# Kernel tuning notes

Hardware: AMD Instinct MI355X
Metric: run time of the kernel (lower is better)

Reference implementation:

```python
import jax, jax.numpy as jnp
import numpy as np

DIM, HEADS = 1536, 12
HD = DIM // HEADS            # 128 head dim
C = HD // 2                  # 64 complex (pair) dim
C0 = C - 2 * (C // 3)        # 22 (temporal axis)
C1 = C // 3                  # 21 (each spatial axis)
MAX_POS = 1024
F_, H_, W_ = 9, 22, 22
SEQ = F_ * H_ * W_           # 4356
NCLASS = 2
EPS = 1e-6


def _rope_tables():
    # Wan rope_params: theta = 10000, per-axis half-dims C0, C1, C1.
    def ang(half):
        inv = 1.0 / (10000.0 ** (np.arange(0, 2 * half, 2) / (2 * half)))
        return np.outer(np.arange(MAX_POS), inv)
    a = np.concatenate([ang(C0), ang(C1), ang(C1)], axis=1)  # [MAX_POS, C]
    return jnp.asarray(np.cos(a), jnp.float32), jnp.asarray(np.sin(a), jnp.float32)


def setup_inputs() -> dict:
    key = jax.random.key(0)
    ks = jax.random.split(key, 6)
    s = 1.0 / np.sqrt(DIM)
    def lin(k):
        k1, k2 = jax.random.split(k)
        return (jax.random.uniform(k1, (DIM, DIM), jnp.float32, -s, s),
                jax.random.uniform(k2, (DIM,), jnp.float32, -s, s))
    Wq, bq = lin(ks[0]); Wk, bk = lin(ks[1]); Wv, bv = lin(ks[2]); Wo, bo = lin(ks[3])
    fc, fs = _rope_tables()
    masks = (jax.random.uniform(ks[4], (NCLASS, H_ * W_)) < 0.5).astype(jnp.float32)
    x = jax.random.normal(ks[5], (1, SEQ, DIM), jnp.float32)
    return {"x": x, "Wq": Wq, "bq": bq, "Wk": Wk, "bk": bk, "Wv": Wv, "bv": bv,
            "Wo": Wo, "bo": bo, "gq": jnp.ones((DIM,), jnp.float32),
            "gk": jnp.ones((DIM,), jnp.float32), "freqs_cos": fc, "freqs_sin": fs,
            "ref_target_masks": masks, "f": F_, "h": H_, "w": W_}


def _rmsnorm(x, g):
    return x * jax.lax.rsqrt(jnp.mean(x * x, axis=-1, keepdims=True) + EPS) * g


def _grid_cs(tab, f, h, w):
    # per-position (f,h,w) rope table -> [f*h*w, C]
    p0 = jnp.broadcast_to(tab[:f, None, None, :C0], (f, h, w, C0))
    p1 = jnp.broadcast_to(tab[None, :h, None, C0:C0 + C1], (f, h, w, C1))
    p2 = jnp.broadcast_to(tab[None, None, :w, C0 + C1:], (f, h, w, C1))
    return jnp.concatenate([p0, p1, p2], axis=-1).reshape(f * h * w, C)


def _rope(x, cos, sin):
    # x: [b,s,n,d]; pairs are interleaved along d (view_as_complex semantics)
    b, s, n, d = x.shape
    xr = x.reshape(b, s, n, d // 2, 2)
    a, bi = xr[..., 0], xr[..., 1]
    cos = cos[None, :, None, :]
    sin = sin[None, :, None, :]
    out = jnp.stack([a * cos - bi * sin, a * sin + bi * cos], axis=-1)
    return out.reshape(b, s, n, d)


def reference(x, Wq, bq, Wk, bk, Wv, bv, Wo, bo, gq, gk, freqs_cos, freqs_sin,
              ref_target_masks, f, h, w):
    b, s, _ = x.shape
    n, d = HEADS, HD
    q = _rmsnorm(x @ Wq.T + bq, gq).reshape(b, s, n, d)
    k = _rmsnorm(x @ Wk.T + bk, gk).reshape(b, s, n, d)
    v = (x @ Wv.T + bv).reshape(b, s, n, d)
    cos = _grid_cs(freqs_cos, f, h, w)
    sin = _grid_cs(freqs_sin, f, h, w)
    q = _rope(q, cos, sin)
    k = _rope(k, cos, sin)
    scale = 1.0 / np.sqrt(d).astype(np.float32)
    # full (window_size == (-1,-1)) attention; seq_lens == s so k_lens mask is identity
    scores = jnp.einsum('bsnd,btnd->bnst', q, k) * scale
    p = jax.nn.softmax(scores, axis=-1)
    o = jnp.einsum('bnst,btnd->bsnd', p, v).reshape(b, s, n * d)
    out = o @ Wo.T + bo
    # aux attention map vs reference-frame keys (first h*w spatial tokens), no-grad path
    xs = h * w
    ref_k = k[:, :xs]
    s2 = jnp.einsum('bsnd,btnd->bnst', q * scale, ref_k)
    p2 = jax.nn.softmax(s2, axis=-1)                       # [b,n,s,xs]
    m = ref_target_masks                                   # [c,xs]
    maps = jnp.einsum('bnst,ct->cbns', p2, m) / jnp.sum(m, axis=-1)[:, None, None, None]
    attn_map = maps.mean(axis=2).reshape(-1, s)            # mean over heads -> [c*b, s]
    return out, attn_map
```

## Files before the change

### kernel.cpp

```cpp
#include <hip/hip_runtime.h>
#include <hip/hip_bf16.h>
#include <math.h>

constexpr int SEQ   = 4356;
constexpr int DIM   = 1536;
constexpr int HEADS = 12;
constexpr int HD    = 128;
constexpr int CH    = 64;
constexpr int C0c   = 22;
constexpr int C1c   = 21;
constexpr int WWc   = 22;
constexpr int HHWW  = 484;
constexpr int XS    = 484;
constexpr int KVB   = 64;
constexpr int NT    = (SEQ + KVB - 1) / KVB;
constexpr int SEQP  = NT * KVB;
constexpr size_t SD = (size_t)SEQ * DIM;

typedef float f32x4 __attribute__((ext_vector_type(4)));
typedef short bf16x8 __attribute__((ext_vector_type(8)));
typedef short bf16x4 __attribute__((ext_vector_type(4)));

__device__ inline unsigned short f2bf(float f) {
  union { float f; unsigned u; } x; x.f = f;
  return (unsigned short)((x.u + 0x7FFFu + ((x.u >> 16) & 1u)) >> 16);
}

#define GLD16(g, l)                                                                        \
  __builtin_amdgcn_global_load_lds((const __attribute__((address_space(1))) unsigned*)    \
                                       (const void*)(g),                                  \
                                   (__attribute__((address_space(3))) unsigned*)(void*)(l),\
                                   16, 0, 0)

__global__ __launch_bounds__(256) void prep_kernel(const float* __restrict__ mask,
                                                   float* __restrict__ amap,
                                                   float* __restrict__ cnt,
                                                   float4* __restrict__ msk4) {
  int t = threadIdx.x;
  for (int i = t; i < 2 * SEQ; i += 256) amap[i] = 0.f;
  for (int i = t; i < 512; i += 256) {
    float4 v;
    v.x = (i < XS) ? mask[i] : 0.f;
    v.y = (i < XS) ? mask[XS + i] : 0.f;
    v.z = (i < XS) ? 1.f : 0.f;
    v.w = 0.f;
    msk4[i] = v;
  }
  float c0 = 0.f, c1 = 0.f;
  for (int i = t; i < XS; i += 256) { c0 += mask[i]; c1 += mask[XS + i]; }
  __shared__ float red0[256];
  __shared__ float red1[256];
  red0[t] = c0; red1[t] = c1;
  __syncthreads();
  for (int off = 128; off > 0; off >>= 1) {
    if (t < off) { red0[t] += red0[t + off]; red1[t] += red1[t + off]; }
    __syncthreads();
  }
  if (t == 0) { cnt[0] = red0[0]; cnt[1] = red1[0]; }
}

__global__ __launch_bounds__(256) void padzero(unsigned short* __restrict__ vt) {
  const int pad = SEQP - SEQ;
  const int total = DIM * pad;
  for (int i = blockIdx.x * 256 + threadIdx.x; i < total; i += gridDim.x * 256) {
    const int d = i / pad, c = i - d * pad;
    vt[(size_t)d * SEQP + SEQ + c] = 0;
  }
}

__global__ __launch_bounds__(256) void to_bf16(const float* __restrict__ in,
                                               unsigned short* __restrict__ out, int n4) {
  for (int i = blockIdx.x * 256 + threadIdx.x; i < n4; i += gridDim.x * 256) {
    const float4 v = ((const float4*)in)[i];
    ushort4 o;
    o.x = f2bf(v.x); o.y = f2bf(v.y); o.z = f2bf(v.z); o.w = f2bf(v.w);
    ((ushort4*)out)[i] = o;
  }
}

__global__ __launch_bounds__(256) void to_bf16_w(const float* __restrict__ W0, const float* __restrict__ W1,
                                                 const float* __restrict__ W2, const float* __restrict__ W3,
                                                 unsigned short* __restrict__ o0, unsigned short* __restrict__ o1,
                                                 unsigned short* __restrict__ o2, unsigned short* __restrict__ o3,
                                                 int n4) {
  const int z = blockIdx.z;
  const float* in = (z == 0) ? W0 : (z == 1) ? W1 : (z == 2) ? W2 : W3;
  unsigned short* out = (z == 0) ? o0 : (z == 1) ? o1 : (z == 2) ? o2 : o3;
  for (int i = blockIdx.x * 256 + threadIdx.x; i < n4; i += gridDim.x * 256) {
    const float4 v = ((const float4*)in)[i];
    ushort4 o;
    o.x = f2bf(v.x); o.y = f2bf(v.y); o.z = f2bf(v.z); o.w = f2bf(v.w);
    ((ushort4*)out)[i] = o;
  }
}

__global__ __launch_bounds__(256) void gemm_qkv(const unsigned short* __restrict__ A,
                                                const unsigned short* __restrict__ B0,
                                                const unsigned short* __restrict__ B1,
                                                const unsigned short* __restrict__ B2,
                                                const float* __restrict__ bq,
                                                const float* __restrict__ bk,
                                                const float* __restrict__ bv,
                                                float* __restrict__ o0,
                                                float* __restrict__ o1,
                                                unsigned short* __restrict__ vtout,
                                                int M) {
  __shared__ unsigned short As[128 * 64];
  __shared__ unsigned short Bs[128 * 64];
  const int z = blockIdx.z;
  const unsigned short* B = (z == 0) ? B0 : (z == 1) ? B1 : B2;
  const float* bias = (z == 0) ? bq : (z == 1) ? bk : bv;
  const int t    = threadIdx.x;
  const int lane = t & 63;
  const int w    = t >> 6;
  const int wr   = w >> 1, wc = w & 1;
  const int bm = blockIdx.x * 128, bn = blockIdx.y * 128;
  const int lq = lane & 15, lg = lane >> 4;
  f32x4 acc[4][4] = {};
  for (int k0 = 0; k0 < DIM; k0 += 64) {
#pragma unroll
    for (int i = 0; i < 4; ++i) {
      const int idx = i * 256 + t;
      const int row = idx >> 3;
      const int c8  = (idx & 7) * 8;
      const int ga  = min(bm + row, M - 1);
      GLD16(A + (size_t)ga * DIM + k0 + c8, As + idx * 8);
      const int gb  = bn + row;
      GLD16(B + (size_t)gb * DIM + k0 + c8, Bs + idx * 8);
    }
    __syncthreads();
#pragma unroll
    for (int kk = 0; kk < 2; ++kk) {
      bf16x8 af[4], bf[4];
#pragma unroll
      for (int m = 0; m < 4; ++m)
        af[m] = *(const bf16x8*)(As + (wr * 64 + m * 16 + lq) * 64 + kk * 32 + lg * 8);
#pragma unroll
      for (int n = 0; n < 4; ++n)
        bf[n] = *(const bf16x8*)(Bs + (wc * 64 + n * 16 + lq) * 64 + kk * 32 + lg * 8);
#pragma unroll
      for (int m = 0; m < 4; ++m)
#pragma unroll
        for (int n = 0; n < 4; ++n)
          acc[m][n] = __builtin_amdgcn_mfma_f32_16x16x32_bf16(af[m], bf[n], acc[m][n], 0, 0, 0);
    }
    __syncthreads();
  }
#pragma unroll
  for (int n = 0; n < 4; ++n) {
    const int col = bn + wc * 64 + n * 16 + lq;
    const float bv2 = bias[col];
#pragma unroll
    for (int m = 0; m < 4; ++m) {
      const int rm = bm + wr * 64 + m * 16 + lg * 4;
      if (z < 2) {
        float* C = (z == 0) ? o0 : o1;
#pragma unroll
        for (int r = 0; r < 4; ++r) {
          const int row = rm + r;
          if (row < M) C[(size_t)row * DIM + col] = acc[m][n][r] + bv2;
        }
      } else {
        if (rm < M) {
          bf16x4 o;
#pragma unroll
          for (int r = 0; r < 4; ++r) o[r] = (short)f2bf(acc[m][n][r] + bv2);
          *(bf16x4*)(vtout + (size_t)col * SEQP + rm) = o;
        }
      }
    }
  }
}

__global__ __launch_bounds__(256) void gemm_mfma(const unsigned short* __restrict__ A,
                                                 const unsigned short* __restrict__ B,
                                                 const float* __restrict__ bias,
                                                 float* __restrict__ C, int M) {
  __shared__ unsigned short As[128 * 64];
  __shared__ unsigned short Bs[128 * 64];
  const int t    = threadIdx.x;
  const int lane = t & 63;
  const int w    = t >> 6;
  const int wr   = w >> 1, wc = w & 1;
  const int bm = blockIdx.x * 128, bn = blockIdx.y * 128;
  const int lq = lane & 15, lg = lane >> 4;
  f32x4 acc[4][4] = {};
  for (int k0 = 0; k0 < DIM; k0 += 64) {
#pragma unroll
    for (int i = 0; i < 4; ++i) {
      const int idx = i * 256 + t;
      const int row = idx >> 3;
      const int c8  = (idx & 7) * 8;
      const int ga  = min(bm + row, M - 1);
      GLD16(A + (size_t)ga * DIM + k0 + c8, As + idx * 8);
      const int gb  = bn + row;
      GLD16(B + (size_t)gb * DIM + k0 + c8, Bs + idx * 8);
    }
    __syncthreads();
#pragma unroll
    for (int kk = 0; kk < 2; ++kk) {
      bf16x8 af[4], bf[4];
#pragma unroll
      for (int m = 0; m < 4; ++m)
        af[m] = *(const bf16x8*)(As + (wr * 64 + m * 16 + lq) * 64 + kk * 32 + lg * 8);
#pragma unroll
      for (int n = 0; n < 4; ++n)
        bf[n] = *(const bf16x8*)(Bs + (wc * 64 + n * 16 + lq) * 64 + kk * 32 + lg * 8);
#pragma unroll
      for (int m = 0; m < 4; ++m)
#pragma unroll
        for (int n = 0; n < 4; ++n)
          acc[m][n] = __builtin_amdgcn_mfma_f32_16x16x32_bf16(af[m], bf[n], acc[m][n], 0, 0, 0);
    }
    __syncthreads();
  }
#pragma unroll
  for (int n = 0; n < 4; ++n) {
    const int col = bn + wc * 64 + n * 16 + lq;
    const float bv = bias[col];
#pragma unroll
    for (int m = 0; m < 4; ++m) {
      const int rm = bm + wr * 64 + m * 16 + lg * 4;
#pragma unroll
      for (int r = 0; r < 4; ++r) {
        const int row = rm + r;
        if (row < M) C[(size_t)row * DIM + col] = acc[m][n][r] + bv;
      }
    }
  }
}

__global__ __launch_bounds__(256) void rms_rope_b(const float* __restrict__ y,
                                                  const float* __restrict__ g,
                                                  const float* __restrict__ fcos,
                                                  const float* __restrict__ fsin,
                                                  float scale,
                                                  unsigned short* __restrict__ outb) {
  const int s = blockIdx.x;
  const float* row = y + (size_t)s * DIM;
  const int t = threadIdx.x;
  float ss = 0.f;
  for (int i = t; i < DIM / 4; i += 256) {
    const float4 v = ((const float4*)row)[i];
    ss += v.x * v.x + v.y * v.y + v.z * v.z + v.w * v.w;
  }
#pragma unroll
  for (int off = 1; off < 64; off <<= 1) ss += __shfl_xor(ss, off);
  __shared__ float wred[4];
  if ((t & 63) == 0) wred[t >> 6] = ss;
  __syncthreads();
  const float tot = wred[0] + wred[1] + wred[2] + wred[3];
  const float rs = rsqrtf(tot * (1.0f / DIM) + 1e-6f);
  const int fi  = s / HHWW;
  const int rem = s - fi * HHWW;
  const int hi  = rem / WWc;
  const int wi  = rem - hi * WWc;
  for (int p = t; p < DIM / 2; p += 256) {
    const int head = p >> 6;
    const int c    = p & 63;
    const int idx  = head * HD + 2 * c;
    const int trow = (c < C0c) ? fi : ((c < C0c + C1c) ? hi : wi);
    const float co = fcos[trow * CH + c];
    const float si = fsin[trow * CH + c];
    const float a  = row[idx] * rs * g[idx];
    const float b  = row[idx + 1] * rs * g[idx + 1];
    ushort2 pr;
    pr.x = f2bf((a * co - b * si) * scale);
    pr.y = f2bf((a * si + b * co) * scale);
    *(ushort2*)(outb + (size_t)s * DIM + idx) = pr;
  }
}

#define TILE_BODY(KB_, MAP_, LAST_, PRE_)                                               \
  {                                                                                     \
    const int kb_ = (KB_);                                                              \
    f32x4 sacc[4] = {};                                                                 \
    _Pragma("unroll")                                                                   \
    for (int kbi = 0; kbi < 4; ++kbi) {                                                 \
      const int krow = kbi * 16 + lq;                                                   \
      _Pragma("unroll")                                                                 \
      for (int c = 0; c < 4; ++c) {                                                     \
        const bf16x8 kf = *(const bf16x8*)((char*)Ks + krow * 256 +                     \
                            (((c * 4 + lg) ^ (krow & 7)) * 16));                        \
        sacc[kbi] = __builtin_amdgcn_mfma_f32_16x16x32_bf16(kf, qf[c], sacc[kbi], 0, 0, 0); \
      }                                                                                 \
    }                                                                                   \
    if (PRE_) {                                                                         \
      const int kbn = kb_ + KVB;                                                        \
      _Pragma("unroll")                                                                 \
      for (int j = 0; j < 4; ++j) {                                                     \
        const int ck = t + j * 256;                                                     \
        const int kr = ck >> 4, ks2 = ck & 15;                                          \
        stK[j] = *(const bf16x8*)(kh + (size_t)min(kbn + kr, SEQ - 1) * DIM + ks2 * 8); \
        const int vd = ck >> 3, vs2 = ck & 7;                                           \
        stV[j] = *(const bf16x8*)(vh + (size_t)vd * SEQP + kbn + vs2 * 8);              \
      }                                                                                 \
    }                                                                                   \
    float sv[16];                                                                       \
    float mt = -1e30f;                                                                  \
    _Pragma("unroll")                                                                   \
    for (int i = 0; i < 16; ++i) {                                                      \
      float v = sacc[i >> 2][i & 3];                                                    \
      if (LAST_) {                                                                      \
        const int key = kb_ + (i >> 2) * 16 + lg * 4 + (i & 3);                         \
        if (key >= SEQ) v = -1e30f;                                                     \
      }                                                                                 \
      sv[i] = v;                                                                        \
      mt = fmaxf(mt, v);                                                                \
    }                                                                                   \
    mt = fmaxf(mt, __shfl_xor(mt, 16));                                                 \
    mt = fmaxf(mt, __shfl_xor(mt, 32));                                                 \
    const bool need = __any(mt > m_run + 8.f);                                          \
    if (need) {                                                                         \
      const float m_new = fmaxf(m_run, mt);                                             \
      const float alpha = __expf(m_run - m_new);                                        \
      m_run = m_new;                                                                    \
      l_run *= alpha;                                                                   \
      _Pragma("unroll")                                                                 \
      for (int db = 0; db < 8; ++db) {                                                  \
        acc[db][0] *= alpha; acc[db][1] *= alpha;                                       \
        acc[db][2] *= alpha; acc[db][3] *= alpha;                                       \
      }                                                                                 \
      if (MAP_) { d2 *= alpha; n0 *= alpha; n1 *= alpha; }                              \
    }                                                                                   \
    float ps = 0.f;                                                                     \
    _Pragma("unroll")                                                                   \
    for (int i = 0; i < 16; ++i) { sv[i] = __expf(sv[i] - m_run); ps += sv[i]; }        \
    ps += __shfl_xor(ps, 16);                                                           \
    ps += __shfl_xor(ps, 32);                                                           \
    l_run += ps;                                                                        \
    if (MAP_) {                                                                         \
      _Pragma("unroll")                                                                 \
      for (int i = 0; i < 16; ++i) {                                                    \
        const int key = kb_ + (i >> 2) * 16 + lg * 4 + (i & 3);                         \
        const float4 mv = Msk[key];                                                     \
        n0 = fmaf(sv[i], mv.x, n0);                                                     \
        n1 = fmaf(sv[i], mv.y, n1);                                                     \
        d2 = fmaf(sv[i], mv.z, d2);                                                     \
      }                                                                                 \
    }                                                                                   \
    _Pragma("unroll")                                                                   \
    for (int kbi = 0; kbi < 4; ++kbi) {                                                 \
      unsigned r0, r1;                                                                  \
      asm("v_cvt_pk_bf16_f32 %0, %1, %2" : "=v"(r0) : "v"(sv[kbi * 4 + 0]), "v"(sv[kbi * 4 + 1])); \
      asm("v_cvt_pk_bf16_f32 %0, %1, %2" : "=v"(r1) : "v"(sv[kbi * 4 + 2]), "v"(sv[kbi * 4 + 3])); \
      uint2 pw; pw.x = r0; pw.y = r1;                                                   \
      *(uint2*)&P[lq][kbi * 16 + lg * 4] = pw;                                          \
    }                                                                                   \
    _Pragma("unroll")                                                                   \
    for (int kk = 0; kk < 2; ++kk) {                                                    \
      const bf16x8 pf = *(const bf16x8*)&P[lq][kk * 32 + lg * 8];                       \
      _Pragma("unroll")                                                                 \
      for (int db = 0; db < 8; ++db) {                                                  \
        const int vd = db * 16 + lq;                                                    \
        const bf16x8 vf = *(const bf16x8*)((char*)Vs + vd * 128 +                       \
                            (((kk * 4 + lg) ^ (vd & 7)) * 16));                         \
        acc[db] = __builtin_amdgcn_mfma_f32_16x16x32_bf16(vf, pf, acc[db], 0, 0, 0);    \
      }                                                                                 \
    }                                                                                   \
    if (PRE_) {                                                                         \
      __syncthreads();                                                                  \
      _Pragma("unroll")                                                                 \
      for (int j = 0; j < 4; ++j) {                                                     \
        const int ck = t + j * 256;                                                     \
        const int kr = ck >> 4, ks2 = ck & 15;                                          \
        *(bf16x8*)((char*)Ks + kr * 256 + ((ks2 ^ (kr & 7)) * 16)) = stK[j];            \
        const int vd = ck >> 3, vs2 = ck & 7;                                           \
        *(bf16x8*)((char*)Vs + vd * 128 + ((vs2 ^ (vd & 7)) * 16)) = stV[j];            \
      }                                                                                 \
      __syncthreads();                                                                  \
    }                                                                                   \
  }

__global__ __launch_bounds__(256) void flash_mfma(const unsigned short* __restrict__ qbuf,
                                                  const unsigned short* __restrict__ kbuf,
                                                  const unsigned short* __restrict__ vt,
                                                  const float4* __restrict__ msk4,
                                                  const float* __restrict__ cnt,
                                                  unsigned short* __restrict__ ob,
                                                  float* __restrict__ amap) {
  const int h    = blockIdx.y;
  const int t    = threadIdx.x;
  const int w    = t >> 6;
  const int lane = t & 63;
  const int lq   = lane & 15, lg = lane >> 4;
  const int qbase = blockIdx.x * 64 + w * 16;

  __shared__ __align__(16) unsigned short Ks[64 * 128];
  __shared__ __align__(16) unsigned short Vs[128 * 64];
  __shared__ __align__(16) unsigned short Plds[4][16][72];
  __shared__ float4 Msk[512];
  unsigned short (*P)[72] = Plds[w];

  const unsigned short* kh = kbuf + h * HD;
  const unsigned short* vh = vt + (size_t)(h * HD) * SEQP;

  for (int i = t; i < 512; i += 256) Msk[i] = msk4[i];

  const int qsrc = min(qbase + lq, SEQ - 1);
  bf16x8 qf[4];
#pragma unroll
  for (int c = 0; c < 4; ++c)
    qf[c] = *(const bf16x8*)(qbuf + (size_t)qsrc * DIM + h * HD + c * 32 + lg * 8);

  f32x4 acc[8] = {};
  float m_run = -1e30f, l_run = 0.f;
  float d2 = 0.f, n0 = 0.f, n1 = 0.f;

  bf16x8 stK[4], stV[4];
#pragma unroll
  for (int j = 0; j < 4; ++j) {
    const int ck = t + j * 256;
    const int kr = ck >> 4, ks2 = ck & 15;
    stK[j] = *(const bf16x8*)(kh + (size_t)min(kr, SEQ - 1) * DIM + ks2 * 8);
    const int vd = ck >> 3, vs2 = ck & 7;
    stV[j] = *(const bf16x8*)(vh + (size_t)vd * SEQP + vs2 * 8);
  }
#pragma unroll
  for (int j = 0; j < 4; ++j) {
    const int ck = t + j * 256;
    const int kr = ck >> 4, ks2 = ck & 15;
    *(bf16x8*)((char*)Ks + kr * 256 + ((ks2 ^ (kr & 7)) * 16)) = stK[j];
    const int vd = ck >> 3, vs2 = ck & 7;
    *(bf16x8*)((char*)Vs + vd * 128 + ((vs2 ^ (vd & 7)) * 16)) = stV[j];
  }
  __syncthreads();

  for (int tile = 0; tile < 8; ++tile)          TILE_BODY(tile * KVB, true,  false, true);
  for (int tile = 8; tile < NT - 1; ++tile)     TILE_BODY(tile * KVB, false, false, true);
  TILE_BODY((NT - 1) * KVB, false, true, false);

  const int qrow = qbase + lq;
  if (qrow < SEQ) {
    const float inv = 1.f / l_run;
#pragma unroll
    for (int db = 0; db < 8; ++db) {
      bf16x4 o;
#pragma unroll
      for (int r = 0; r < 4; ++r) o[r] = (short)f2bf(acc[db][r] * inv);
      *(bf16x4*)(ob + (size_t)qrow * DIM + h * HD + db * 16 + lg * 4) = o;
    }
  }
  d2 += __shfl_xor(d2, 16); d2 += __shfl_xor(d2, 32);
  n0 += __shfl_xor(n0, 16); n0 += __shfl_xor(n0, 32);
  n1 += __shfl_xor(n1, 16); n1 += __shfl_xor(n1, 32);
  if (lane < 16 && qrow < SEQ) {
    const float invd = 1.f / (d2 * (float)HEADS);
    atomicAdd(&amap[qrow],       n0 * invd / cnt[0]);
    atomicAdd(&amap[SEQ + qrow], n1 * invd / cnt[1]);
  }
}

extern "C" void kernel_launch(void* const* d_in, const int* in_sizes, int n_in,
                              void* d_out, int out_size, void* d_ws, size_t ws_size,
                              hipStream_t stream) {
  const float* x    = (const float*)d_in[0];
  const float* Wq   = (const float*)d_in[1];
  const float* bq   = (const float*)d_in[2];
  const float* Wk   = (const float*)d_in[3];
  const float* bk   = (const float*)d_in[4];
  const float* Wv   = (const float*)d_in[5];
  const float* bv   = (const float*)d_in[6];
  const float* Wo   = (const float*)d_in[7];
  const float* bo   = (const float*)d_in[8];
  const float* gq   = (const float*)d_in[9];
  const float* gk   = (const float*)d_in[10];
  const float* fc   = (const float*)d_in[11];
  const float* fs   = (const float*)d_in[12];
  const float* mask = (const float*)d_in[13];

  float* out  = (float*)d_out;
  float* amap = out + SD;
  float* f32a = out;

  float* f32b        = (float*)d_ws;
  unsigned short* xb = (unsigned short*)(f32b + SD);
  unsigned short* qb = xb + SD;
  unsigned short* kb = qb + SD;
  unsigned short* vt = kb + SD;
  unsigned short* wqb = vt + (size_t)DIM * SEQP;
  unsigned short* wkb = wqb + (size_t)DIM * DIM;
  unsigned short* wvb = wkb + (size_t)DIM * DIM;
  unsigned short* wob = wvb + (size_t)DIM * DIM;
  float4* msk4 = (float4*)(wob + (size_t)DIM * DIM);
  float* cnt  = (float*)(msk4 + 512);
  unsigned short* ob = (unsigned short*)f32b;

  prep_kernel<<<1, 256, 0, stream>>>(mask, amap, cnt, msk4);
  padzero<<<64, 256, 0, stream>>>(vt);
  to_bf16<<<2048, 256, 0, stream>>>(x, xb, (int)(SD / 4));
  constexpr int W4 = DIM * DIM / 4;
  to_bf16_w<<<dim3(512, 1, 4), 256, 0, stream>>>(Wq, Wk, Wv, Wo, wqb, wkb, wvb, wob, W4);

  const dim3 gg((SEQ + 127) / 128, DIM / 128, 3);
  gemm_qkv<<<gg, 256, 0, stream>>>(xb, wqb, wkb, wvb, bq, bk, bv, f32a, f32b, vt, SEQ);

  const float scale = 0.08838834764831845f;
  rms_rope_b<<<SEQ, 256, 0, stream>>>(f32a, gq, fc, fs, scale, qb);
  rms_rope_b<<<SEQ, 256, 0, stream>>>(f32b, gk, fc, fs, 1.0f, kb);

  const dim3 fg((SEQ + 63) / 64, HEADS);
  flash_mfma<<<fg, 256, 0, stream>>>(qb, kb, vt, msk4, cnt, ob, amap);

  const dim3 go((SEQ + 127) / 128, DIM / 128);
  gemm_mfma<<<go, 256, 0, stream>>>(ob, wob, bo, out, SEQ);
}
```

Before: 468.2 us.

## Halve flash KV tile to 32, pad V rows, raise occupancy, merge rms_rope launches

The flash attention KV tile shrinks from 64 to 32 keys, which halves the K/V shared memory and staging registers. The V tile switches from an XOR swizzle to padded rows (stride 40), and launch bounds now request 4 blocks per SM so more waves can hide latency. The two rms_rope launches are merged into one 2D grid. The cost is twice as many tile iterations and barriers, and a PV step that issues one MFMA k-chunk per tile instead of two.

```diff
diff --git a/kernel.cpp b/kernel.cpp
--- a/kernel.cpp
+++ b/kernel.cpp
@@ -12,9 +12,10 @@
 constexpr int WWc   = 22;
 constexpr int HHWW  = 484;
 constexpr int XS    = 484;
-constexpr int KVB   = 64;
+constexpr int KVB   = 32;
 constexpr int NT    = (SEQ + KVB - 1) / KVB;
-constexpr int SEQP  = NT * KVB;
+constexpr int SEQP  = 4416;
+constexpr int VP    = 40;
 constexpr size_t SD = (size_t)SEQ * DIM;
 
 typedef float f32x4 __attribute__((ext_vector_type(4)));
@@ -230,12 +231,19 @@
   }
 }
 
-__global__ __launch_bounds__(256) void rms_rope_b(const float* __restrict__ y,
-                                                  const float* __restrict__ g,
-                                                  const float* __restrict__ fcos,
-                                                  const float* __restrict__ fsin,
-                                                  float scale,
-                                                  unsigned short* __restrict__ outb) {
+__global__ __launch_bounds__(256) void rms_rope2(const float* __restrict__ qy,
+                                                 const float* __restrict__ ky,
+                                                 const float* __restrict__ gq,
+                                                 const float* __restrict__ gk,
+                                                 const float* __restrict__ fcos,
+                                                 const float* __restrict__ fsin,
+                                                 unsigned short* __restrict__ qout,
+                                                 unsigned short* __restrict__ kout) {
+  const int z = blockIdx.y;
+  const float* y = z ? ky : qy;
+  const float* g = z ? gk : gq;
+  unsigned short* outb = z ? kout : qout;
+  const float scale = z ? 1.0f : 0.08838834764831845f;
   const int s = blockIdx.x;
   const float* row = y + (size_t)s * DIM;
   const int t = threadIdx.x;
@@ -274,9 +282,9 @@
 #define TILE_BODY(KB_, MAP_, LAST_, PRE_)                                               \
   {                                                                                     \
     const int kb_ = (KB_);                                                              \
-    f32x4 sacc[4] = {};                                                                 \
+    f32x4 sacc[2] = {};                                                                 \
     _Pragma("unroll")                                                                   \
-    for (int kbi = 0; kbi < 4; ++kbi) {                                                 \
+    for (int kbi = 0; kbi < 2; ++kbi) {                                                 \
       const int krow = kbi * 16 + lq;                                                   \
       _Pragma("unroll")                                                                 \
       for (int c = 0; c < 4; ++c) {                                                     \
@@ -288,18 +296,18 @@
     if (PRE_) {                                                                         \
       const int kbn = kb_ + KVB;                                                        \
       _Pragma("unroll")                                                                 \
-      for (int j = 0; j < 4; ++j) {                                                     \
+      for (int j = 0; j < 2; ++j) {                                                     \
         const int ck = t + j * 256;                                                     \
         const int kr = ck >> 4, ks2 = ck & 15;                                          \
         stK[j] = *(const bf16x8*)(kh + (size_t)min(kbn + kr, SEQ - 1) * DIM + ks2 * 8); \
-        const int vd = ck >> 3, vs2 = ck & 7;                                           \
+        const int vd = ck >> 2, vs2 = ck & 3;                                           \
         stV[j] = *(const bf16x8*)(vh + (size_t)vd * SEQP + kbn + vs2 * 8);              \
       }                                                                                 \
     }                                                                                   \
-    float sv[16];                                                                       \
+    float sv[8];                                                                        \
     float mt = -1e30f;                                                                  \
     _Pragma("unroll")                                                                   \
-    for (int i = 0; i < 16; ++i) {                                                      \
+    for (int i = 0; i < 8; ++i) {                                                       \
       float v = sacc[i >> 2][i & 3];                                                    \
       if (LAST_) {                                                                      \
         const int key = kb_ + (i >> 2) * 16 + lg * 4 + (i & 3);                         \
@@ -325,13 +333,13 @@
     }                                                                                   \
     float ps = 0.f;                                                                     \
     _Pragma("unroll")                                                                   \
-    for (int i = 0; i < 16; ++i) { sv[i] = __expf(sv[i] - m_run); ps += sv[i]; }        \
+    for (int i = 0; i < 8; ++i) { sv[i] = __expf(sv[i] - m_run); ps += sv[i]; }         \
     ps += __shfl_xor(ps, 16);                                                           \
     ps += __shfl_xor(ps, 32);                                                           \
     l_run += ps;                                                                        \
     if (MAP_) {                                                                         \
       _Pragma("unroll")                                                                 \
-      for (int i = 0; i < 16; ++i) {                                                    \
+      for (int i = 0; i < 8; ++i) {                                                     \
         const int key = kb_ + (i >> 2) * 16 + lg * 4 + (i & 3);                         \
         const float4 mv = Msk[key];                                                     \
         n0 = fmaf(sv[i], mv.x, n0);                                                     \
@@ -340,45 +348,42 @@
       }                                                                                 \
     }                                                                                   \
     _Pragma("unroll")                                                                   \
-    for (int kbi = 0; kbi < 4; ++kbi) {                                                 \
+    for (int kbi = 0; kbi < 2; ++kbi) {                                                 \
       unsigned r0, r1;                                                                  \
       asm("v_cvt_pk_bf16_f32 %0, %1, %2" : "=v"(r0) : "v"(sv[kbi * 4 + 0]), "v"(sv[kbi * 4 + 1])); \
       asm("v_cvt_pk_bf16_f32 %0, %1, %2" : "=v"(r1) : "v"(sv[kbi * 4 + 2]), "v"(sv[kbi * 4 + 3])); \
       uint2 pw; pw.x = r0; pw.y = r1;                                                   \
       *(uint2*)&P[lq][kbi * 16 + lg * 4] = pw;                                          \
     }                                                                                   \
-    _Pragma("unroll")                                                                   \
-    for (int kk = 0; kk < 2; ++kk) {                                                    \
-      const bf16x8 pf = *(const bf16x8*)&P[lq][kk * 32 + lg * 8];                       \
+    {                                                                                   \
+      const bf16x8 pf = *(const bf16x8*)&P[lq][lg * 8];                                 \
       _Pragma("unroll")                                                                 \
       for (int db = 0; db < 8; ++db) {                                                  \
-        const int vd = db * 16 + lq;                                                    \
-        const bf16x8 vf = *(const bf16x8*)((char*)Vs + vd * 128 +                       \
-                            (((kk * 4 + lg) ^ (vd & 7)) * 16));                         \
+        const bf16x8 vf = *(const bf16x8*)(Vs + (db * 16 + lq) * VP + lg * 8);          \
         acc[db] = __builtin_amdgcn_mfma_f32_16x16x32_bf16(vf, pf, acc[db], 0, 0, 0);    \
       }                                                                                 \
     }                                                                                   \
     if (PRE_) {                                                                         \
       __syncthreads();                                                                  \
       _Pragma("unroll")                                                                 \
-      for (int j = 0; j < 4; ++j) {                                                     \
+      for (int j = 0; j < 2; ++j) {                                                     \
         const int ck = t + j * 256;                                                     \
         const int kr = ck >> 4, ks2 = ck & 15;                                          \
         *(bf16x8*)((char*)Ks + kr * 256 + ((ks2 ^ (kr & 7)) * 16)) = stK[j];            \
-        const int vd = ck >> 3, vs2 = ck & 7;                                           \
-        *(bf16x8*)((char*)Vs + vd * 128 + ((vs2 ^ (vd & 7)) * 16)) = stV[j];            \
+        const int vd = ck >> 2, vs2 = ck & 3;                                           \
+        *(bf16x8*)(Vs + vd * VP + vs2 * 8) = stV[j];                                    \
       }                                                                                 \
       __syncthreads();                                                                  \
     }                                                                                   \
   }
 
-__global__ __launch_bounds__(256) void flash_mfma(const unsigned short* __restrict__ qbuf,
-                                                  const unsigned short* __restrict__ kbuf,
-                                                  const unsigned short* __restrict__ vt,
-                                                  const float4* __restrict__ msk4,
-                                                  const float* __restrict__ cnt,
-                                                  unsigned short* __restrict__ ob,
-                                                  float* __restrict__ amap) {
+__global__ __launch_bounds__(256, 4) void flash_mfma(const unsigned short* __restrict__ qbuf,
+                                                     const unsigned short* __restrict__ kbuf,
+                                                     const unsigned short* __restrict__ vt,
+                                                     const float4* __restrict__ msk4,
+                                                     const float* __restrict__ cnt,
+                                                     unsigned short* __restrict__ ob,
+                                                     float* __restrict__ amap) {
   const int h    = blockIdx.y;
   const int t    = threadIdx.x;
   const int w    = t >> 6;
@@ -386,8 +391,8 @@
   const int lq   = lane & 15, lg = lane >> 4;
   const int qbase = blockIdx.x * 64 + w * 16;
 
-  __shared__ __align__(16) unsigned short Ks[64 * 128];
-  __shared__ __align__(16) unsigned short Vs[128 * 64];
+  __shared__ __align__(16) unsigned short Ks[KVB * 128];
+  __shared__ __align__(16) unsigned short Vs[128 * VP];
   __shared__ __align__(16) unsigned short Plds[4][16][72];
   __shared__ float4 Msk[512];
   unsigned short (*P)[72] = Plds[w];
@@ -407,27 +412,27 @@
   float m_run = -1e30f, l_run = 0.f;
   float d2 = 0.f, n0 = 0.f, n1 = 0.f;
 
-  bf16x8 stK[4], stV[4];
-#pragma unroll
-  for (int j = 0; j < 4; ++j) {
+  bf16x8 stK[2], stV[2];
+#pragma unroll
+  for (int j = 0; j < 2; ++j) {
     const int ck = t + j * 256;
     const int kr = ck >> 4, ks2 = ck & 15;
     stK[j] = *(const bf16x8*)(kh + (size_t)min(kr, SEQ - 1) * DIM + ks2 * 8);
-    const int vd = ck >> 3, vs2 = ck & 7;
+    const int vd = ck >> 2, vs2 = ck & 3;
     stV[j] = *(const bf16x8*)(vh + (size_t)vd * SEQP + vs2 * 8);
   }
 #pragma unroll
-  for (int j = 0; j < 4; ++j) {
+  for (int j = 0; j < 2; ++j) {
     const int ck = t + j * 256;
     const int kr = ck >> 4, ks2 = ck & 15;
     *(bf16x8*)((char*)Ks + kr * 256 + ((ks2 ^ (kr & 7)) * 16)) = stK[j];
-    const int vd = ck >> 3, vs2 = ck & 7;
-    *(bf16x8*)((char*)Vs + vd * 128 + ((vs2 ^ (vd & 7)) * 16)) = stV[j];
+    const int vd = ck >> 2, vs2 = ck & 3;
+    *(bf16x8*)(Vs + vd * VP + vs2 * 8) = stV[j];
   }
   __syncthreads();
 
-  for (int tile = 0; tile < 8; ++tile)          TILE_BODY(tile * KVB, true,  false, true);
-  for (int tile = 8; tile < NT - 1; ++tile)     TILE_BODY(tile * KVB, false, false, true);
+  for (int tile = 0; tile < 16; ++tile)         TILE_BODY(tile * KVB, true,  false, true);
+  for (int tile = 16; tile < NT - 1; ++tile)    TILE_BODY(tile * KVB, false, false, true);
   TILE_BODY((NT - 1) * KVB, false, true, false);
 
   const int qrow = qbase + lq;
@@ -495,9 +500,7 @@
   const dim3 gg((SEQ + 127) / 128, DIM / 128, 3);
   gemm_qkv<<<gg, 256, 0, stream>>>(xb, wqb, wkb, wvb, bq, bk, bv, f32a, f32b, vt, SEQ);
 
-  const float scale = 0.08838834764831845f;
-  rms_rope_b<<<SEQ, 256, 0, stream>>>(f32a, gq, fc, fs, scale, qb);
-  rms_rope_b<<<SEQ, 256, 0, stream>>>(f32b, gk, fc, fs, 1.0f, kb);
+  rms_rope2<<<dim3(SEQ, 2), 256, 0, stream>>>(f32a, f32b, gq, gk, fc, fs, qb, kb);
 
   const dim3 fg((SEQ + 63) / 64, HEADS);
   flash_mfma<<<fg, 256, 0, stream>>>(qb, kb, vt, msk4, cnt, ob, amap);
```

Result: no change. 467.2 us (-0.2%).
